# Kernel optimization log

Hardware: AMD Instinct MI355X
Metric: run time of the kernel (lower is better)

Reference implementation:

```python
import jax, jax.numpy as jnp
import numpy as np


def setup_inputs() -> dict:
    key = jax.random.key(0)
    ks = jax.random.split(key, 9)
    B, T, D, U = 512, 1024, 64, 128
    inp = {
        'inputs': jax.random.normal(ks[0], (B, T, D), dtype=jnp.float32),
        'W_f': jax.random.normal(ks[1], (D, U), dtype=jnp.float32) * 0.05,
        'U_f': jax.random.normal(ks[2], (U, U), dtype=jnp.float32) * 0.05,
        'b_f': jnp.zeros((U,), dtype=jnp.float32),
        'W_i': jax.random.normal(ks[3], (D, U), dtype=jnp.float32) * 0.05,
        'U_i': jax.random.normal(ks[4], (U, U), dtype=jnp.float32) * 0.05,
        'b_i': jnp.zeros((U,), dtype=jnp.float32),
        'W_c': jax.random.normal(ks[5], (D, U), dtype=jnp.float32) * 0.05,
        'U_c': jax.random.normal(ks[6], (U, U), dtype=jnp.float32) * 0.05,
        'b_c': jnp.zeros((U,), dtype=jnp.float32),
        'W_o': jax.random.normal(ks[7], (D, U), dtype=jnp.float32) * 0.05,
        'U_o': jax.random.normal(ks[8], (U, U), dtype=jnp.float32) * 0.05,
        'b_o': jnp.zeros((U,), dtype=jnp.float32),
    }
    return inp


def _lstm(inputs, W_f, U_f, b_f, W_i, U_i, b_i, W_c, U_c, b_c, W_o, U_o, b_o):
    B, T, D = inputs.shape
    U = W_f.shape[1]
    # Precompute all input-to-gate projections in one batched GEMM per gate: [B,T,U]
    xf = jnp.einsum('btd,du->btu', inputs, W_f) + b_f
    xi = jnp.einsum('btd,du->btu', inputs, W_i) + b_i
    xc = jnp.einsum('btd,du->btu', inputs, W_c) + b_c
    xo = jnp.einsum('btd,du->btu', inputs, W_o) + b_o
    # time-major stacked gate inputs: [T, B, 4, U]
    xg = jnp.stack([xf, xi, xc, xo], axis=2).transpose(1, 0, 2, 3)
    # concatenated recurrent weights: [U, 4U]
    U_all = jnp.concatenate([U_f, U_i, U_c, U_o], axis=1)

    def step(carry, x_t):
        h, c = carry
        # x_t: [B, 4, U]
        rec = (h @ U_all).reshape(B, 4, U)
        g = x_t + rec
        f = jax.nn.sigmoid(g[:, 0])
        i = jax.nn.sigmoid(g[:, 1])
        c_tilde = jnp.tanh(g[:, 2])
        o = jax.nn.sigmoid(g[:, 3])
        c_new = f * c + i * c_tilde
        h_new = o * jnp.tanh(c_new)
        return (h_new, c_new), None

    h0 = jnp.zeros((B, U), dtype=inputs.dtype)
    c0 = jnp.zeros((B, U), dtype=inputs.dtype)
    (h, c), _ = jax.lax.scan(step, (h0, c0), xg)
    return h


def reference(inputs, W_f, U_f, b_f, W_i, U_i, b_i, W_c, U_c, b_c, W_o, U_o, b_o):
    return _lstm(inputs, W_f, U_f, b_f, W_i, U_i, b_i, W_c, U_c, b_c, W_o, U_o, b_o)
```

## Files before the change

### kernel.cpp

```cpp
#include <hip/hip_runtime.h>
#include <stdint.h>


typedef __attribute__((ext_vector_type(8))) short short8;
typedef __attribute__((ext_vector_type(4))) float floatx4;
typedef __attribute__((ext_vector_type(4))) int   intx4;
typedef __attribute__((ext_vector_type(8))) int   intx8;

#define B_SZ   512
#define T_SZ   1024
#define D_SZ   64
#define U_SZ   128
#define ROWS   2
#define NBLK   (B_SZ / ROWS)
#define NTHR   512
#define A1STRB 160
#define GXSTR  524

__device__ __forceinline__ short f2bf(float f) {
    uint32_t u = __builtin_bit_cast(uint32_t, f);
    uint32_t r = (u + 0x7fffu + ((u >> 16) & 1u)) >> 16;
    return (short)r;
}
__device__ __forceinline__ float fsig(float x) {
    return __builtin_amdgcn_rcpf(1.0f + __builtin_amdgcn_exp2f(-1.4426950408889634f * x));
}
__device__ __forceinline__ float ftanh(float x) {
    return 1.0f - 2.0f * __builtin_amdgcn_rcpf(1.0f + __builtin_amdgcn_exp2f(2.8853900817779268f * x));
}
__device__ __forceinline__ void sync_lds() {
    asm volatile("s_waitcnt lgkmcnt(0)\n\ts_barrier" ::: "memory");
}

__global__ __launch_bounds__(NTHR, 2) void lstm_persistent(
    const float* __restrict__ xin,
    const float* __restrict__ Wf, const float* __restrict__ Uf, const float* __restrict__ bfp,
    const float* __restrict__ Wi, const float* __restrict__ Ui, const float* __restrict__ bip,
    const float* __restrict__ Wc, const float* __restrict__ Uc, const float* __restrict__ bcp,
    const float* __restrict__ Wo, const float* __restrict__ Uo, const float* __restrict__ bop,
    float* __restrict__ out)
{
    __shared__ float Gx[2][16 * GXSTR];
    __shared__ __align__(8) char A1[2][2 * A1STRB];

    const int tid  = threadIdx.x;
    const int wave = tid >> 6;
    const int lane = tid & 63;
    const int quad = lane >> 4;
    const int nlo  = lane & 15;
    const int blk  = blockIdx.x;

    const float* Wg[4] = {Wf, Wi, Wc, Wo};
    const float* Ug[4] = {Uf, Ui, Uc, Uo};

    if (wave < 4) {
        const int ti_s = quad & 1;
        const int prow = quad >> 1;
        const int u_s  = 32 * wave + 16 * ti_s + nlo;

        intx8 bU8[4][2];
#pragma unroll
        for (int g = 0; g < 4; ++g)
#pragma unroll
            for (int ti = 0; ti < 2; ++ti) {
                const int uc = 32 * wave + 16 * ti + nlo;
#pragma unroll
                for (int d = 0; d < 8; ++d) {
                    const int k0 = quad * 32 + d * 4;
                    int pk = __builtin_amdgcn_cvt_pk_fp8_f32(
                        Ug[g][(k0 + 0) * U_SZ + uc], Ug[g][(k0 + 1) * U_SZ + uc], 0, 0);
                    pk = __builtin_amdgcn_cvt_pk_fp8_f32(
                        Ug[g][(k0 + 2) * U_SZ + uc], Ug[g][(k0 + 3) * U_SZ + uc], pk, 1);
                    bU8[g][ti][d] = pk;
                }
            }
        const floatx4 bias4 = {bfp[u_s], bip[u_s], bcp[u_s], bop[u_s]};
        float c_st = 0.0f;

        for (int i = tid; i < 2 * 2 * A1STRB; i += 256) ((char*)A1)[i] = 0;
        __syncthreads();

        for (int g = 0; g < 128; ++g) {
            const float* GxR = &Gx[g & 1][0];
#pragma unroll
            for (int j = 0; j < 8; ++j) {
                const char* ap = &A1[j & 1][(nlo & 1) * A1STRB + quad * 32];
                intx4 alo = *(const intx4*)(ap);
                intx4 ahi = *(const intx4*)(ap + 16);
                floatx4 gx = *(const floatx4*)&GxR[(2 * j + prow) * GXSTR + 4 * u_s];
                intx8 a8 = {alo.x, alo.y, alo.z, alo.w, ahi.x, ahi.y, ahi.z, ahi.w};
                gx += bias4;

                floatx4 acc0[4], acc1[4];
#pragma unroll
                for (int gt = 0; gt < 4; ++gt) {
                    floatx4 z = (floatx4){0.f, 0.f, 0.f, 0.f};
                    acc0[gt] = __builtin_amdgcn_mfma_scale_f32_16x16x128_f8f6f4(
                        a8, bU8[gt][0], z, 0, 0, 0, 0x7f7f7f7f, 0, 0x7f7f7f7f);
                }
#pragma unroll
                for (int gt = 0; gt < 4; ++gt) {
                    floatx4 z = (floatx4){0.f, 0.f, 0.f, 0.f};
                    acc1[gt] = __builtin_amdgcn_mfma_scale_f32_16x16x128_f8f6f4(
                        a8, bU8[gt][1], z, 0, 0, 0, 0x7f7f7f7f, 0, 0x7f7f7f7f);
                }

                float gA0 = (prow ? acc0[0][1] : acc0[0][0]) + gx[0];
                float gA1 = (prow ? acc0[1][1] : acc0[1][0]) + gx[1];
                float gA2 = (prow ? acc0[2][1] : acc0[2][0]) + gx[2];
                float gA3 = (prow ? acc0[3][1] : acc0[3][0]) + gx[3];
                float fA = fsig(gA0), iA = fsig(gA1), cAt = ftanh(gA2), oA = fsig(gA3);
                float cA = fA * c_st + iA * cAt;
                float hA = oA * ftanh(cA);

                float gB0 = (prow ? acc1[0][1] : acc1[0][0]) + gx[0];
                float gB1 = (prow ? acc1[1][1] : acc1[1][0]) + gx[1];
                float gB2 = (prow ? acc1[2][1] : acc1[2][0]) + gx[2];
                float gB3 = (prow ? acc1[3][1] : acc1[3][0]) + gx[3];
                float fB = fsig(gB0), iB = fsig(gB1), cBt = ftanh(gB2), oB = fsig(gB3);
                float cB = fB * c_st + iB * cBt;
                float hB = oB * ftanh(cB);

                c_st = ti_s ? cB : cA;
                float h = ti_s ? hB : hA;

                if (g == 127 && j == 7) {
                    out[(size_t)(blk * ROWS + prow) * U_SZ + u_s] = h;
                } else {
                    int pk = __builtin_amdgcn_cvt_pk_fp8_f32(h, h, 0, 0);
                    A1[(j & 1) ^ 1][prow * A1STRB + u_s] = (char)(pk & 0xff);
                }
                sync_lds();
            }
        }
    } else {
        const int p = wave - 4;
        const int brow  = nlo & 1;
        const int t_off = nlo >> 1;

        short8 bWp[8][2];
#pragma unroll
        for (int tau = 0; tau < 8; ++tau) {
            const int gt = tau >> 1;
            const int uc = 16 * (2 * p + (tau & 1)) + nlo;
#pragma unroll
            for (int kt = 0; kt < 2; ++kt)
#pragma unroll
                for (int jj = 0; jj < 8; ++jj) {
                    int k = kt * 32 + quad * 8 + jj;
                    bWp[tau][kt][jj] = f2bf(Wg[gt][k * U_SZ + uc]);
                }
        }

        const float* xg = xin + ((size_t)(blk * ROWS + brow) * T_SZ) * D_SZ + quad * 8;

        float4 p0 = *(const float4*)(xg + (size_t)t_off * D_SZ + 0);
        float4 p1 = *(const float4*)(xg + (size_t)t_off * D_SZ + 4);
        float4 p2 = *(const float4*)(xg + (size_t)t_off * D_SZ + 32);
        float4 p3 = *(const float4*)(xg + (size_t)t_off * D_SZ + 36);
        float4 q0 = *(const float4*)(xg + (size_t)(8 + t_off) * D_SZ + 0);
        float4 q1 = *(const float4*)(xg + (size_t)(8 + t_off) * D_SZ + 4);
        float4 q2 = *(const float4*)(xg + (size_t)(8 + t_off) * D_SZ + 32);
        float4 q3 = *(const float4*)(xg + (size_t)(8 + t_off) * D_SZ + 36);

        short8 xa0 = {f2bf(p0.x), f2bf(p0.y), f2bf(p0.z), f2bf(p0.w),
                      f2bf(p1.x), f2bf(p1.y), f2bf(p1.z), f2bf(p1.w)};
        short8 xa1 = {f2bf(p2.x), f2bf(p2.y), f2bf(p2.z), f2bf(p2.w),
                      f2bf(p3.x), f2bf(p3.y), f2bf(p3.z), f2bf(p3.w)};
#pragma unroll
        for (int tau = 0; tau < 8; ++tau) {
            const int gt = tau >> 1;
            const int uc = 16 * (2 * p + (tau & 1)) + nlo;
            floatx4 acc = (floatx4){0.f, 0.f, 0.f, 0.f};
            acc = __builtin_amdgcn_mfma_f32_16x16x32_bf16(xa0, bWp[tau][0], acc, 0, 0, 0);
            acc = __builtin_amdgcn_mfma_f32_16x16x32_bf16(xa1, bWp[tau][1], acc, 0, 0, 0);
#pragma unroll
            for (int r = 0; r < 4; ++r)
                Gx[0][(quad * 4 + r) * GXSTR + 4 * uc + gt] = acc[r];
        }
        xa0 = (short8){f2bf(q0.x), f2bf(q0.y), f2bf(q0.z), f2bf(q0.w),
                       f2bf(q1.x), f2bf(q1.y), f2bf(q1.z), f2bf(q1.w)};
        xa1 = (short8){f2bf(q2.x), f2bf(q2.y), f2bf(q2.z), f2bf(q2.w),
                       f2bf(q3.x), f2bf(q3.y), f2bf(q3.z), f2bf(q3.w)};
        float4 xq0 = *(const float4*)(xg + (size_t)(16 + t_off) * D_SZ + 0);
        float4 xq1 = *(const float4*)(xg + (size_t)(16 + t_off) * D_SZ + 4);
        float4 xq2 = *(const float4*)(xg + (size_t)(16 + t_off) * D_SZ + 32);
        float4 xq3 = *(const float4*)(xg + (size_t)(16 + t_off) * D_SZ + 36);
        __syncthreads();

        short8 xn0 = xa0, xn1 = xa1;
        for (int g = 0; g < 128; ++g) {
            float* GxW = &Gx[(g + 1) & 1][0];
#pragma unroll
            for (int j = 0; j < 8; ++j) {
                if (j == 0 && g <= 125) {
                    xn0 = (short8){f2bf(xq0.x), f2bf(xq0.y), f2bf(xq0.z), f2bf(xq0.w),
                                   f2bf(xq1.x), f2bf(xq1.y), f2bf(xq1.z), f2bf(xq1.w)};
                    xn1 = (short8){f2bf(xq2.x), f2bf(xq2.y), f2bf(xq2.z), f2bf(xq2.w),
                                   f2bf(xq3.x), f2bf(xq3.y), f2bf(xq3.z), f2bf(xq3.w)};
                }
                if (j == 1 && g <= 124) {
                    const float* b = xg + (size_t)(8 * (g + 3) + t_off) * D_SZ;
                    xq0 = *(const float4*)(b + 0);
                    xq1 = *(const float4*)(b + 4);
                    xq2 = *(const float4*)(b + 32);
                    xq3 = *(const float4*)(b + 36);
                }
                if (g < 127) {
                    const int gt = j >> 1;
                    const int uc = 16 * (2 * p + (j & 1)) + nlo;
                    floatx4 acc = (floatx4){0.f, 0.f, 0.f, 0.f};
                    acc = __builtin_amdgcn_mfma_f32_16x16x32_bf16(xa0, bWp[j][0], acc, 0, 0, 0);
                    acc = __builtin_amdgcn_mfma_f32_16x16x32_bf16(xa1, bWp[j][1], acc, 0, 0, 0);
#pragma unroll
                    for (int r = 0; r < 4; ++r)
                        GxW[(quad * 4 + r) * GXSTR + 4 * uc + gt] = acc[r];
                }
                sync_lds();
            }
            xa0 = xn0; xa1 = xn1;
        }
    }
}

extern "C" void kernel_launch(void* const* d_in, const int* in_sizes, int n_in,
                              void* d_out, int out_size, void* d_ws, size_t ws_size,
                              hipStream_t stream) {
    (void)in_sizes; (void)n_in; (void)d_ws; (void)ws_size; (void)out_size;
    const float* xin = (const float*)d_in[0];
    const float* Wf  = (const float*)d_in[1];
    const float* Uf  = (const float*)d_in[2];
    const float* bf  = (const float*)d_in[3];
    const float* Wi  = (const float*)d_in[4];
    const float* Ui  = (const float*)d_in[5];
    const float* bi  = (const float*)d_in[6];
    const float* Wc  = (const float*)d_in[7];
    const float* Uc  = (const float*)d_in[8];
    const float* bc  = (const float*)d_in[9];
    const float* Wo  = (const float*)d_in[10];
    const float* Uo  = (const float*)d_in[11];
    const float* bo  = (const float*)d_in[12];
    float* out = (float*)d_out;

    hipLaunchKernelGGL(lstm_persistent, dim3(NBLK), dim3(NTHR), 0, stream,
                       xin, Wf, Uf, bf, Wi, Ui, bi, Wc, Uc, bc, Wo, Uo, bo, out);
}
```

Measured before the change: 567.1 us.

## Halve recurrent gate math, move bias to producer, use packed bf16 converts

```diff
diff --git a/kernel.cpp b/kernel.cpp
--- a/kernel.cpp
+++ b/kernel.cpp
@@ -21,6 +21,15 @@
     uint32_t u = __builtin_bit_cast(uint32_t, f);
     uint32_t r = (u + 0x7fffu + ((u >> 16) & 1u)) >> 16;
     return (short)r;
+}
+__device__ __forceinline__ int cvt2bf(float lo, float hi) {
+    int r;
+    asm("v_cvt_pk_bf16_f32 %0, %1, %2" : "=v"(r) : "v"(lo), "v"(hi));
+    return r;
+}
+__device__ __forceinline__ short8 pk8(float4 a, float4 b) {
+    intx4 t = {cvt2bf(a.x, a.y), cvt2bf(a.z, a.w), cvt2bf(b.x, b.y), cvt2bf(b.z, b.w)};
+    return __builtin_bit_cast(short8, t);
 }
 __device__ __forceinline__ float fsig(float x) {
     return __builtin_amdgcn_rcpf(1.0f + __builtin_amdgcn_exp2f(-1.4426950408889634f * x));
@@ -52,8 +61,10 @@
 
     const float* Wg[4] = {Wf, Wi, Wc, Wo};
     const float* Ug[4] = {Uf, Ui, Uc, Uo};
+    const float* Bg[4] = {bfp, bip, bcp, bop};
 
     if (wave < 4) {
+        __builtin_amdgcn_s_setprio(1);
         const int ti_s = quad & 1;
         const int prow = quad >> 1;
         const int u_s  = 32 * wave + 16 * ti_s + nlo;
@@ -74,7 +85,6 @@
                     bU8[g][ti][d] = pk;
                 }
             }
-        const floatx4 bias4 = {bfp[u_s], bip[u_s], bcp[u_s], bop[u_s]};
         float c_st = 0.0f;
 
         for (int i = tid; i < 2 * 2 * A1STRB; i += 256) ((char*)A1)[i] = 0;
@@ -84,12 +94,11 @@
             const float* GxR = &Gx[g & 1][0];
 #pragma unroll
             for (int j = 0; j < 8; ++j) {
-                const char* ap = &A1[j & 1][(nlo & 1) * A1STRB + quad * 32];
+                const char* ap = &A1[j & 1][(nlo >> 3) * A1STRB + quad * 32];
                 intx4 alo = *(const intx4*)(ap);
                 intx4 ahi = *(const intx4*)(ap + 16);
                 floatx4 gx = *(const floatx4*)&GxR[(2 * j + prow) * GXSTR + 4 * u_s];
                 intx8 a8 = {alo.x, alo.y, alo.z, alo.w, ahi.x, ahi.y, ahi.z, ahi.w};
-                gx += bias4;
 
                 floatx4 acc0[4], acc1[4];
 #pragma unroll
@@ -105,24 +114,14 @@
                         a8, bU8[gt][1], z, 0, 0, 0, 0x7f7f7f7f, 0, 0x7f7f7f7f);
                 }
 
-                float gA0 = (prow ? acc0[0][1] : acc0[0][0]) + gx[0];
-                float gA1 = (prow ? acc0[1][1] : acc0[1][0]) + gx[1];
-                float gA2 = (prow ? acc0[2][1] : acc0[2][0]) + gx[2];
-                float gA3 = (prow ? acc0[3][1] : acc0[3][0]) + gx[3];
-                float fA = fsig(gA0), iA = fsig(gA1), cAt = ftanh(gA2), oA = fsig(gA3);
-                float cA = fA * c_st + iA * cAt;
-                float hA = oA * ftanh(cA);
-
-                float gB0 = (prow ? acc1[0][1] : acc1[0][0]) + gx[0];
-                float gB1 = (prow ? acc1[1][1] : acc1[1][0]) + gx[1];
-                float gB2 = (prow ? acc1[2][1] : acc1[2][0]) + gx[2];
-                float gB3 = (prow ? acc1[3][1] : acc1[3][0]) + gx[3];
-                float fB = fsig(gB0), iB = fsig(gB1), cBt = ftanh(gB2), oB = fsig(gB3);
-                float cB = fB * c_st + iB * cBt;
-                float hB = oB * ftanh(cB);
-
-                c_st = ti_s ? cB : cA;
-                float h = ti_s ? hB : hA;
+                float g0 = (ti_s ? acc1[0][0] : acc0[0][0]) + gx[0];
+                float g1 = (ti_s ? acc1[1][0] : acc0[1][0]) + gx[1];
+                float g2 = (ti_s ? acc1[2][0] : acc0[2][0]) + gx[2];
+                float g3 = (ti_s ? acc1[3][0] : acc0[3][0]) + gx[3];
+                float fg = fsig(g0), ig = fsig(g1), ctl = ftanh(g2), og = fsig(g3);
+                float c = fg * c_st + ig * ctl;
+                float h = og * ftanh(c);
+                c_st = c;
 
                 if (g == 127 && j == 7) {
                     out[(size_t)(blk * ROWS + prow) * U_SZ + u_s] = h;
@@ -139,10 +138,12 @@
         const int t_off = nlo >> 1;
 
         short8 bWp[8][2];
+        float  bw[8];
 #pragma unroll
         for (int tau = 0; tau < 8; ++tau) {
             const int gt = tau >> 1;
             const int uc = 16 * (2 * p + (tau & 1)) + nlo;
+            bw[tau] = Bg[gt][uc];
 #pragma unroll
             for (int kt = 0; kt < 2; ++kt)
 #pragma unroll
@@ -163,10 +164,8 @@
         float4 q2 = *(const float4*)(xg + (size_t)(8 + t_off) * D_SZ + 32);
         float4 q3 = *(const float4*)(xg + (size_t)(8 + t_off) * D_SZ + 36);
 
-        short8 xa0 = {f2bf(p0.x), f2bf(p0.y), f2bf(p0.z), f2bf(p0.w),
-                      f2bf(p1.x), f2bf(p1.y), f2bf(p1.z), f2bf(p1.w)};
-        short8 xa1 = {f2bf(p2.x), f2bf(p2.y), f2bf(p2.z), f2bf(p2.w),
-                      f2bf(p3.x), f2bf(p3.y), f2bf(p3.z), f2bf(p3.w)};
+        short8 xa0 = pk8(p0, p1);
+        short8 xa1 = pk8(p2, p3);
 #pragma unroll
         for (int tau = 0; tau < 8; ++tau) {
             const int gt = tau >> 1;
@@ -176,12 +175,10 @@
             acc = __builtin_amdgcn_mfma_f32_16x16x32_bf16(xa1, bWp[tau][1], acc, 0, 0, 0);
 #pragma unroll
             for (int r = 0; r < 4; ++r)
-                Gx[0][(quad * 4 + r) * GXSTR + 4 * uc + gt] = acc[r];
-        }
-        xa0 = (short8){f2bf(q0.x), f2bf(q0.y), f2bf(q0.z), f2bf(q0.w),
-                       f2bf(q1.x), f2bf(q1.y), f2bf(q1.z), f2bf(q1.w)};
-        xa1 = (short8){f2bf(q2.x), f2bf(q2.y), f2bf(q2.z), f2bf(q2.w),
-                       f2bf(q3.x), f2bf(q3.y), f2bf(q3.z), f2bf(q3.w)};
+                Gx[0][(quad * 4 + r) * GXSTR + 4 * uc + gt] = acc[r] + bw[tau];
+        }
+        xa0 = pk8(q0, q1);
+        xa1 = pk8(q2, q3);
         float4 xq0 = *(const float4*)(xg + (size_t)(16 + t_off) * D_SZ + 0);
         float4 xq1 = *(const float4*)(xg + (size_t)(16 + t_off) * D_SZ + 4);
         float4 xq2 = *(const float4*)(xg + (size_t)(16 + t_off) * D_SZ + 32);
@@ -194,10 +191,8 @@
 #pragma unroll
             for (int j = 0; j < 8; ++j) {
                 if (j == 0 && g <= 125) {
-                    xn0 = (short8){f2bf(xq0.x), f2bf(xq0.y), f2bf(xq0.z), f2bf(xq0.w),
-                                   f2bf(xq1.x), f2bf(xq1.y), f2bf(xq1.z), f2bf(xq1.w)};
-                    xn1 = (short8){f2bf(xq2.x), f2bf(xq2.y), f2bf(xq2.z), f2bf(xq2.w),
-                                   f2bf(xq3.x), f2bf(xq3.y), f2bf(xq3.z), f2bf(xq3.w)};
+                    xn0 = pk8(xq0, xq1);
+                    xn1 = pk8(xq2, xq3);
                 }
                 if (j == 1 && g <= 124) {
                     const float* b = xg + (size_t)(8 * (g + 3) + t_off) * D_SZ;
@@ -207,14 +202,13 @@
                     xq3 = *(const float4*)(b + 36);
                 }
                 if (g < 127) {
-                    const int gt = j >> 1;
                     const int uc = 16 * (2 * p + (j & 1)) + nlo;
                     floatx4 acc = (floatx4){0.f, 0.f, 0.f, 0.f};
                     acc = __builtin_amdgcn_mfma_f32_16x16x32_bf16(xa0, bWp[j][0], acc, 0, 0, 0);
                     acc = __builtin_amdgcn_mfma_f32_16x16x32_bf16(xa1, bWp[j][1], acc, 0, 0, 0);
 #pragma unroll
                     for (int r = 0; r < 4; ++r)
-                        GxW[(quad * 4 + r) * GXSTR + 4 * uc + gt] = acc[r];
+                        GxW[(quad * 4 + r) * GXSTR + 4 * uc + (j >> 1)] = acc[r] + bw[j];
                 }
                 sync_lds();
             }
```

Measured after the change: 545.6 us. 1.04x faster.
